# Performance work log

Hardware: AMD Instinct MI355X
Metric: run time of the kernel (lower is better)

The kernel has to match this reference:

```python
import jax, jax.numpy as jnp
import numpy as np

D = 1024
H = 16
HD = D // H  # 64
S = 2048
B = 1


def setup_inputs() -> dict:
    key = jax.random.key(0)
    ks = jax.random.split(key, 6)
    return {
        "GLO": jax.random.normal(ks[0], (B, S, D), dtype=jnp.float32),
        "LOC": jax.random.normal(ks[1], (B, S, D), dtype=jnp.float32),
        "W_q": jax.random.normal(ks[2], (H, D, HD), dtype=jnp.float32),
        "W_k": jax.random.normal(ks[3], (H, D, HD), dtype=jnp.float32),
        "W_v": jax.random.normal(ks[4], (H, D, HD), dtype=jnp.float32),
        "W_o": jax.random.normal(ks[5], (H * HD, D), dtype=jnp.float32),
    }


def _cross_attn(q_src, kv_src, W_q, W_k, W_v, W_o):
    # q_src: [B,Sq,D], kv_src: [B,Sk,D]
    b, sq, _ = q_src.shape
    Q = jnp.einsum('bsd,hde->bhse', q_src, W_q)   # [B,H,Sq,hd]
    K = jnp.einsum('bsd,hde->bhse', kv_src, W_k)  # [B,H,Sk,hd]
    V = jnp.einsum('bsd,hde->bhse', kv_src, W_v)  # [B,H,Sk,hd]
    scores = jnp.einsum('bhqe,bhke->bhqk', Q, K) / jnp.sqrt(jnp.float32(HD))
    weights = jax.nn.softmax(scores, axis=-1)
    out = jnp.einsum('bhqk,bhke->bhqe', weights, V)  # [B,H,Sq,hd]
    # Faithful to torch .view (raw memory reinterpretation, no head transpose)
    out = out.reshape(b, sq, H * HD)
    return out @ W_o  # [B,Sq,D]


def reference(GLO, LOC, W_q, W_k, W_v, W_o):
    GLO_prime = _cross_attn(GLO, LOC, W_q, W_k, W_v, W_o)
    LOC_prime = _cross_attn(LOC, GLO, W_q, W_k, W_v, W_o)
    return (GLO_prime, LOC_prime)
```

## Files before the change

### kernel.cpp

```cpp
#include <hip/hip_runtime.h>
#include <math.h>

#define S_LEN 2048
#define D_DIM 1024
#define NH 16
#define HD 64

typedef __attribute__((ext_vector_type(8))) short bf16x8;
typedef __attribute__((ext_vector_type(4))) float f32x4;

#define MFMA(a, b, c) __builtin_amdgcn_mfma_f32_16x16x32_bf16((a), (b), (c), 0, 0, 0)

__device__ __forceinline__ unsigned short f2bf(float x) {
    unsigned int u = __float_as_uint(x);
    u = (u + 0x7FFFu + ((u >> 16) & 1u)) >> 16;
    return (unsigned short)u;
}
__device__ __forceinline__ float bf2f(unsigned short b) {
    return __uint_as_float(((unsigned int)b) << 16);
}
__device__ __forceinline__ void gl_lds16(const void* g, void* l) {
    __builtin_amdgcn_global_load_lds((const __attribute__((address_space(1))) unsigned int*)g,
                                     (__attribute__((address_space(3))) unsigned int*)l, 16, 0, 0);
}


__global__ __launch_bounds__(256) void prep(const float* __restrict__ GLO,
                                            const float* __restrict__ LOC,
                                            const float* __restrict__ Wq,
                                            const float* __restrict__ Wk,
                                            const float* __restrict__ Wv,
                                            const float* __restrict__ Wo,
                                            unsigned short* __restrict__ Xh,
                                            unsigned short* __restrict__ Xl,
                                            unsigned short* __restrict__ Wqh,
                                            unsigned short* __restrict__ Wql,
                                            unsigned short* __restrict__ Wkh,
                                            unsigned short* __restrict__ Wkl,
                                            unsigned short* __restrict__ Wvt,
                                            unsigned short* __restrict__ Wot) {
    int idx = blockIdx.x * 256 + threadIdx.x;
    if (idx < (1 << 22)) {
        const float* src = (idx & (1 << 21)) ? LOC : GLO;
        float x = src[idx & ((1 << 21) - 1)];
        int r = idx >> 10;
        int k = idx & 1023;
        size_t t = (size_t)(r >> 7) * 131072 + (size_t)(k >> 6) * 8192 + (r & 127) * 64 +
                   ((((k >> 3) & 7) ^ (r & 7)) * 8) + (k & 7);
        unsigned short h = f2bf(x);
        Xh[t] = h;
        Xl[t] = f2bf(x - bf2f(h));
    } else {
        idx -= (1 << 22);
        int sec = idx >> 20;
        int i = idx & 0xFFFFF;
        if (sec < 3) {
            int e = i & 63;
            int d = (i >> 6) & 1023;
            int h = i >> 16;
            float wv = ((sec == 0) ? Wq : (sec == 1) ? Wk : Wv)[h * 65536 + d * 64 + e];
            size_t t = (size_t)h * 65536 + (size_t)(d >> 6) * 4096 + e * 64 +
                       ((((d >> 3) & 7) ^ (e & 7)) * 8) + (d & 7);
            if (sec == 0) {
                wv *= 0.18033688011112042f;
                unsigned short hi = f2bf(wv);
                Wqh[t] = hi;
                Wql[t] = f2bf(wv - bf2f(hi));
            } else if (sec == 1) {
                unsigned short hi = f2bf(wv);
                Wkh[t] = hi;
                Wkl[t] = f2bf(wv - bf2f(hi));
            } else {
                Wvt[t] = f2bf(wv);
            }
        } else {
            int n = i & 1023;
            int k = i >> 10;
            size_t t = (size_t)(n >> 6) * 65536 + (size_t)(k >> 6) * 4096 + (n & 63) * 64 +
                       ((((k >> 3) & 7) ^ (n & 7)) * 8) + (k & 7);
            Wot[t] = f2bf(Wo[k * 1024 + n]);
        }
    }
}

__global__ __launch_bounds__(256) void qkv_proj(const unsigned short* __restrict__ Xh,
                                                const unsigned short* __restrict__ Xl,
                                                const unsigned short* __restrict__ Wqh,
                                                const unsigned short* __restrict__ Wql,
                                                const unsigned short* __restrict__ Wkh,
                                                const unsigned short* __restrict__ Wkl,
                                                const unsigned short* __restrict__ Wvt,
                                                unsigned short* __restrict__ Qh,
                                                unsigned short* __restrict__ Ql,
                                                unsigned short* __restrict__ Kh,
                                                unsigned short* __restrict__ Kl,
                                                unsigned short* __restrict__ Vt) {
    __shared__ unsigned short lds[36864];
    const int bid = blockIdx.x;
    const int mblk = bid & 31;
    const int head = bid >> 5;
    const int tid = threadIdx.x;
    const int lane = tid & 63;
    const int w = tid >> 6;
    const int l15 = lane & 15, quad = lane >> 4;

    f32x4 aq[2][4] = {}, ak[2][4] = {}, av[2][4] = {};
    const size_t abase0 = (size_t)mblk * 131072;
    const size_t bbase0 = (size_t)head * 65536;

    for (int kb = 0; kb < 16; ++kb) {
        __syncthreads();
        {
            const size_t ab = abase0 + (size_t)kb * 8192;
            const size_t bb = bbase0 + (size_t)kb * 4096;
#pragma unroll
            for (int j = 0; j < 4; ++j) {
                int seg = j * 256 + tid;
                gl_lds16(Xh + ab + seg * 8, &lds[seg * 8]);
                gl_lds16(Xl + ab + seg * 8, &lds[8192 + seg * 8]);
            }
#pragma unroll
            for (int j = 0; j < 2; ++j) {
                int seg = j * 256 + tid;
                gl_lds16(Wqh + bb + seg * 8, &lds[16384 + seg * 8]);
                gl_lds16(Wql + bb + seg * 8, &lds[20480 + seg * 8]);
                gl_lds16(Wkh + bb + seg * 8, &lds[24576 + seg * 8]);
                gl_lds16(Wkl + bb + seg * 8, &lds[28672 + seg * 8]);
                gl_lds16(Wvt + bb + seg * 8, &lds[32768 + seg * 8]);
            }
        }
        __syncthreads();

#pragma unroll
        for (int ksub = 0; ksub < 2; ++ksub) {
            bf16x8 ah[2], al8[2];
#pragma unroll
            for (int mt = 0; mt < 2; ++mt) {
                int row = w * 32 + mt * 16 + l15;
                int g = (ksub * 4 + quad) ^ (row & 7);
                ah[mt] = *(const bf16x8*)&lds[row * 64 + g * 8];
                al8[mt] = *(const bf16x8*)&lds[8192 + row * 64 + g * 8];
            }
#pragma unroll
            for (int nt = 0; nt < 4; ++nt) {
                int col = nt * 16 + l15;
                int o = col * 64 + ((ksub * 4 + quad) ^ (col & 7)) * 8;
                bf16x8 bqh = *(const bf16x8*)&lds[16384 + o];
                bf16x8 bql = *(const bf16x8*)&lds[20480 + o];
                bf16x8 bkh = *(const bf16x8*)&lds[24576 + o];
                bf16x8 bkl = *(const bf16x8*)&lds[28672 + o];
                bf16x8 bv = *(const bf16x8*)&lds[32768 + o];
#pragma unroll
                for (int mt = 0; mt < 2; ++mt) {
                    f32x4 a = aq[mt][nt];
                    a = MFMA(ah[mt], bqh, a);
                    a = MFMA(ah[mt], bql, a);
                    a = MFMA(al8[mt], bqh, a);
                    aq[mt][nt] = a;
                    f32x4 b = ak[mt][nt];
                    b = MFMA(ah[mt], bkh, b);
                    b = MFMA(ah[mt], bkl, b);
                    b = MFMA(al8[mt], bkh, b);
                    ak[mt][nt] = b;
                    av[mt][nt] = MFMA(ah[mt], bv, av[mt][nt]);
                }
            }
        }
    }

#pragma unroll
    for (int mt = 0; mt < 2; ++mt) {
        const int rbase = mblk * 128 + w * 32 + mt * 16 + quad * 4;
#pragma unroll
        for (int nt = 0; nt < 4; ++nt) {
            const int col = head * 64 + nt * 16 + l15;
#pragma unroll
            for (int r = 0; r < 4; ++r) {
                size_t a = (size_t)(rbase + r) * D_DIM + col;
                float vq = aq[mt][nt][r];
                unsigned short hq = f2bf(vq);
                Qh[a] = hq;
                Ql[a] = f2bf(vq - bf2f(hq));
                float vk = ak[mt][nt][r];
                unsigned short hk = f2bf(vk);
                Kh[a] = hk;
                Kl[a] = f2bf(vk - bf2f(hk));
            }
            ushort4 vp;
            vp.x = f2bf(av[mt][nt][0]);
            vp.y = f2bf(av[mt][nt][1]);
            vp.z = f2bf(av[mt][nt][2]);
            vp.w = f2bf(av[mt][nt][3]);
            *(ushort4*)(Vt + (size_t)col * (2 * S_LEN) + rbase) = vp;
        }
    }
}

__global__ __launch_bounds__(256) void attn_kernel(const unsigned short* __restrict__ Qh_,
                                                   const unsigned short* __restrict__ Ql_,
                                                   const unsigned short* __restrict__ Kh_,
                                                   const unsigned short* __restrict__ Kl_,
                                                   const unsigned short* __restrict__ Vt_,
                                                   unsigned short* __restrict__ Oatt) {
    __shared__ unsigned short lds[21504];
    const int bid = blockIdx.x;
    const int qblk = bid & 15;
    const int head = (bid >> 4) & 15;
    const int dir = bid >> 8;
    const int src_q = dir, src_kv = 1 - dir;

    const int tid = threadIdx.x;
    const int lane = tid & 63;
    const int w = tid >> 6;
    const int l15 = lane & 15, quad = lane >> 4;
    const int q0w = qblk * 128 + w * 32;

    bf16x8 qh[2][2], ql[2][2];
#pragma unroll
    for (int mt = 0; mt < 2; ++mt) {
        const size_t qrow =
            (size_t)(src_q * S_LEN + q0w + mt * 16 + l15) * D_DIM + head * 64 + quad * 8;
#pragma unroll
        for (int c = 0; c < 2; ++c) {
            qh[mt][c] = *(const bf16x8*)(Qh_ + qrow + c * 32);
            ql[mt][c] = *(const bf16x8*)(Ql_ + qrow + c * 32);
        }
    }

    f32x4 o[2][4] = {};
    float mi[2] = {-1e30f, -1e30f}, li[2] = {0.f, 0.f};
    unsigned short* Pw = lds + 12288 + w * 2304;

    for (int k0 = 0; k0 < S_LEN; k0 += 64) {
        __syncthreads();
        {
            const unsigned short* KhB = Kh_ + (size_t)(src_kv * S_LEN + k0) * D_DIM + head * 64;
            const unsigned short* KlB = Kl_ + (size_t)(src_kv * S_LEN + k0) * D_DIM + head * 64;
            const unsigned short* VB = Vt_ + (size_t)(head * 64) * (2 * S_LEN) + src_kv * S_LEN + k0;
#pragma unroll
            for (int j = 0; j < 2; ++j) {
                int i = j * 256 + tid;
                int row = i >> 3, c16 = i & 7;
                int sc = c16 ^ (row & 7);
                gl_lds16(KhB + (size_t)row * D_DIM + sc * 8, &lds[i * 8]);
                gl_lds16(KlB + (size_t)row * D_DIM + sc * 8, &lds[4096 + i * 8]);
                gl_lds16(VB + (size_t)row * (2 * S_LEN) + sc * 8, &lds[8192 + i * 8]);
            }
        }
        __syncthreads();

        f32x4 sa[2][4];
#pragma unroll
        for (int kt = 0; kt < 4; ++kt) {
            const int row = kt * 16 + l15;
            const int s0 = (quad ^ (row & 7)) * 8;
            const int s1 = ((4 + quad) ^ (row & 7)) * 8;
            bf16x8 kh0 = *(const bf16x8*)&lds[row * 64 + s0];
            bf16x8 kh1 = *(const bf16x8*)&lds[row * 64 + s1];
            bf16x8 kl0 = *(const bf16x8*)&lds[4096 + row * 64 + s0];
            bf16x8 kl1 = *(const bf16x8*)&lds[4096 + row * 64 + s1];
#pragma unroll
            for (int mt = 0; mt < 2; ++mt) {
                f32x4 a = {};
                a = MFMA(kh0, qh[mt][0], a);
                a = MFMA(kh1, qh[mt][1], a);
                a = MFMA(kl0, qh[mt][0], a);
                a = MFMA(kl1, qh[mt][1], a);
                a = MFMA(kh0, ql[mt][0], a);
                a = MFMA(kh1, ql[mt][1], a);
                sa[mt][kt] = a;
            }
        }

#pragma unroll
        for (int mt = 0; mt < 2; ++mt) {
            f32x4 t4 = __builtin_elementwise_max(__builtin_elementwise_max(sa[mt][0], sa[mt][1]),
                                                 __builtin_elementwise_max(sa[mt][2], sa[mt][3]));
            float tm = fmaxf(fmaxf(t4[0], t4[1]), fmaxf(t4[2], t4[3]));
            tm = fmaxf(tm, __shfl_xor(tm, 16, 64));
            tm = fmaxf(tm, __shfl_xor(tm, 32, 64));
            float mn = fmaxf(mi[mt], tm);
            float al = exp2f(mi[mt] - mn);
            mi[mt] = mn;
            const f32x4 mnv = {mn, mn, mn, mn};
            f32x4 rs4 = {};
#pragma unroll
            for (int kt = 0; kt < 4; ++kt) {
                f32x4 p = sa[mt][kt] - mnv;
#pragma unroll
                for (int r = 0; r < 4; ++r) p[r] = exp2f(p[r]);
                rs4 += p;
                unsigned u0 = __float_as_uint(p[0]) + 0x8000u;
                unsigned u1 = __float_as_uint(p[1]) + 0x8000u;
                unsigned u2 = __float_as_uint(p[2]) + 0x8000u;
                unsigned u3 = __float_as_uint(p[3]) + 0x8000u;
                uint2 pk;
                pk.x = __builtin_amdgcn_perm(u1, u0, 0x07060302u);
                pk.y = __builtin_amdgcn_perm(u3, u2, 0x07060302u);
                *(uint2*)&Pw[(mt * 16 + l15) * 72 + kt * 16 + quad * 4] = pk;
            }
            float rs = (rs4[0] + rs4[1]) + (rs4[2] + rs4[3]);
            rs += __shfl_xor(rs, 16, 64);
            rs += __shfl_xor(rs, 32, 64);
            li[mt] = li[mt] * al + rs;
            const f32x4 alv = {al, al, al, al};
#pragma unroll
            for (int et = 0; et < 4; ++et) o[mt][et] *= alv;
        }

#pragma unroll
        for (int c = 0; c < 2; ++c) {
            bf16x8 pf[2];
#pragma unroll
            for (int mt = 0; mt < 2; ++mt)
                pf[mt] = *(const bf16x8*)&Pw[(mt * 16 + l15) * 72 + c * 32 + quad * 8];
#pragma unroll
            for (int et = 0; et < 4; ++et) {
                const int row = et * 16 + l15;
                const int sl = ((c * 4 + quad) ^ (row & 7)) * 8;
                bf16x8 vf = *(const bf16x8*)&lds[8192 + row * 64 + sl];
#pragma unroll
                for (int mt = 0; mt < 2; ++mt) o[mt][et] = MFMA(vf, pf[mt], o[mt][et]);
            }
        }
    }

    const size_t obase = (size_t)(dir * 16 + head) * 131072 + (size_t)l15 * 8192;
#pragma unroll
    for (int mt = 0; mt < 2; ++mt) {
        float rl = __builtin_amdgcn_rcpf(li[mt]);
        const int rowit = qblk * 8 + w * 2 + mt;
#pragma unroll
        for (int et = 0; et < 4; ++et) {
            int g = ((et * 2 + (quad >> 1)) ^ (rowit & 7)) & 7;
            ushort4 pk;
            pk.x = f2bf(o[mt][et][0] * rl);
            pk.y = f2bf(o[mt][et][1] * rl);
            pk.z = f2bf(o[mt][et][2] * rl);
            pk.w = f2bf(o[mt][et][3] * rl);
            *(ushort4*)(Oatt + obase + (size_t)rowit * 64 + g * 8 + (quad & 1) * 4) = pk;
        }
    }
}

__global__ __launch_bounds__(256) void oproj(const unsigned short* __restrict__ Oatt,
                                             const unsigned short* __restrict__ Wot,
                                             float* __restrict__ out) {
    __shared__ unsigned short lds[12288];
    const int bid = blockIdx.x;
    const int nblk = bid & 15;
    const int mblk = bid >> 4;
    const int tid = threadIdx.x;
    const int lane = tid & 63, w = tid >> 6, l15 = lane & 15, quad = lane >> 4;

    f32x4 acc[2][4] = {};
    const size_t abase = (size_t)mblk * 131072;
    const size_t bbase = (size_t)nblk * 65536;
    for (int kb = 0; kb < 16; ++kb) {
        __syncthreads();
#pragma unroll
        for (int j = 0; j < 4; ++j) {
            int seg = j * 256 + tid;
            gl_lds16(Oatt + abase + (size_t)kb * 8192 + seg * 8, &lds[seg * 8]);
        }
#pragma unroll
        for (int j = 0; j < 2; ++j) {
            int seg = j * 256 + tid;
            gl_lds16(Wot + bbase + (size_t)kb * 4096 + seg * 8, &lds[8192 + seg * 8]);
        }
        __syncthreads();
#pragma unroll
        for (int ksub = 0; ksub < 2; ++ksub) {
            bf16x8 a[2];
#pragma unroll
            for (int mt = 0; mt < 2; ++mt) {
                int row = w * 32 + mt * 16 + l15;
                a[mt] = *(const bf16x8*)&lds[row * 64 + (((ksub * 4 + quad) ^ (row & 7)) * 8)];
            }
#pragma unroll
            for (int nt = 0; nt < 4; ++nt) {
                int col = nt * 16 + l15;
                bf16x8 b =
                    *(const bf16x8*)&lds[8192 + col * 64 + (((ksub * 4 + quad) ^ (col & 7)) * 8)];
#pragma unroll
                for (int mt = 0; mt < 2; ++mt) acc[mt][nt] = MFMA(a[mt], b, acc[mt][nt]);
            }
        }
    }
#pragma unroll
    for (int mt = 0; mt < 2; ++mt) {
        const int rbase = mblk * 128 + w * 32 + mt * 16 + quad * 4;
#pragma unroll
        for (int nt = 0; nt < 4; ++nt)
#pragma unroll
            for (int r = 0; r < 4; ++r)
                out[(size_t)(rbase + r) * D_DIM + nblk * 64 + nt * 16 + l15] = acc[mt][nt][r];
    }
}

extern "C" void kernel_launch(void* const* d_in, const int* in_sizes, int n_in, void* d_out,
                              int out_size, void* d_ws, size_t ws_size, hipStream_t stream) {
    const float* GLO = (const float*)d_in[0];
    const float* LOC = (const float*)d_in[1];
    const float* Wq = (const float*)d_in[2];
    const float* Wk = (const float*)d_in[3];
    const float* Wv = (const float*)d_in[4];
    const float* Wo = (const float*)d_in[5];
    float* out = (float*)d_out;

    unsigned short* ws = (unsigned short*)d_ws;
    unsigned short* Xh = ws + 0;
    unsigned short* Xl = ws + 4194304;
    unsigned short* Wqh = ws + 8388608;
    unsigned short* Wql = ws + 9437184;
    unsigned short* Wkh = ws + 10485760;
    unsigned short* Wkl = ws + 11534336;
    unsigned short* Wvt = ws + 12582912;
    unsigned short* Wot = ws + 13631488;
    unsigned short* Qh = ws + 14680064;
    unsigned short* Ql = ws + 18874368;
    unsigned short* Kh = ws + 23068672;
    unsigned short* Kl = ws + 27262976;
    unsigned short* Vt = ws + 31457280;
    unsigned short* Oatt = ws + 35651584;

    prep<<<32768, 256, 0, stream>>>(GLO, LOC, Wq, Wk, Wv, Wo, Xh, Xl, Wqh, Wql, Wkh, Wkl, Wvt, Wot);
    qkv_proj<<<512, 256, 0, stream>>>(Xh, Xl, Wqh, Wql, Wkh, Wkl, Wvt, Qh, Ql, Kh, Kl, Vt);
    attn_kernel<<<512, 256, 0, stream>>>(Qh, Ql, Kh, Kl, Vt, Oatt);
    oproj<<<512, 256, 0, stream>>>(Oatt, Wot, out);
}
```

Baseline: 291.4 us.

## Split attention KV range across two blocks and merge partials in combine kernel

The attention grid doubles so each block handles half of the key/value sequence. Partial outputs plus the row max and sum are written to scratch buffers that reuse the Xh/Xl workspace, and a new combine kernel merges the two halves. The online-softmax rescale is now skipped when no lane's maximum grows, and the P tile in shared memory drops its padding in favour of an XOR swizzle. The split raises the block count from 512 to 1024 to improve occupancy across CUs, at the cost of an extra kernel launch, extra global traffic and an extra bf16 rounding of the partial outputs.

```diff
diff --git a/kernel.cpp b/kernel.cpp
--- a/kernel.cpp
+++ b/kernel.cpp
@@ -196,17 +196,20 @@
     }
 }
 
-__global__ __launch_bounds__(256) void attn_kernel(const unsigned short* __restrict__ Qh_,
-                                                   const unsigned short* __restrict__ Ql_,
-                                                   const unsigned short* __restrict__ Kh_,
-                                                   const unsigned short* __restrict__ Kl_,
-                                                   const unsigned short* __restrict__ Vt_,
-                                                   unsigned short* __restrict__ Oatt) {
-    __shared__ unsigned short lds[21504];
+__global__ __launch_bounds__(256, 4) void attn_kernel(const unsigned short* __restrict__ Qh_,
+                                                      const unsigned short* __restrict__ Ql_,
+                                                      const unsigned short* __restrict__ Kh_,
+                                                      const unsigned short* __restrict__ Kl_,
+                                                      const unsigned short* __restrict__ Vt_,
+                                                      unsigned short* __restrict__ Opart0,
+                                                      unsigned short* __restrict__ Opart1,
+                                                      float* __restrict__ MlL) {
+    __shared__ unsigned short lds[20480];
     const int bid = blockIdx.x;
     const int qblk = bid & 15;
     const int head = (bid >> 4) & 15;
-    const int dir = bid >> 8;
+    const int dir = (bid >> 8) & 1;
+    const int ks = bid >> 9;
     const int src_q = dir, src_kv = 1 - dir;
 
     const int tid = threadIdx.x;
@@ -229,9 +232,10 @@
 
     f32x4 o[2][4] = {};
     float mi[2] = {-1e30f, -1e30f}, li[2] = {0.f, 0.f};
-    unsigned short* Pw = lds + 12288 + w * 2304;
-
-    for (int k0 = 0; k0 < S_LEN; k0 += 64) {
+    unsigned short* Pw = lds + 12288 + w * 2048;
+
+    const int kbeg = ks * 1024;
+    for (int k0 = kbeg; k0 < kbeg + 1024; k0 += 64) {
         __syncthreads();
         {
             const unsigned short* KhB = Kh_ + (size_t)(src_kv * S_LEN + k0) * D_DIM + head * 64;
@@ -279,9 +283,16 @@
             float tm = fmaxf(fmaxf(t4[0], t4[1]), fmaxf(t4[2], t4[3]));
             tm = fmaxf(tm, __shfl_xor(tm, 16, 64));
             tm = fmaxf(tm, __shfl_xor(tm, 32, 64));
-            float mn = fmaxf(mi[mt], tm);
-            float al = exp2f(mi[mt] - mn);
-            mi[mt] = mn;
+            if (__ballot(tm > mi[mt])) {
+                float mn = fmaxf(mi[mt], tm);
+                float al = exp2f(mi[mt] - mn);
+                mi[mt] = mn;
+                li[mt] *= al;
+                const f32x4 alv = {al, al, al, al};
+#pragma unroll
+                for (int et = 0; et < 4; ++et) o[mt][et] *= alv;
+            }
+            const float mn = mi[mt];
             const f32x4 mnv = {mn, mn, mn, mn};
             f32x4 rs4 = {};
 #pragma unroll
@@ -297,15 +308,13 @@
                 uint2 pk;
                 pk.x = __builtin_amdgcn_perm(u1, u0, 0x07060302u);
                 pk.y = __builtin_amdgcn_perm(u3, u2, 0x07060302u);
-                *(uint2*)&Pw[(mt * 16 + l15) * 72 + kt * 16 + quad * 4] = pk;
+                int g = (kt * 2 + (quad >> 1)) ^ (l15 & 7);
+                *(uint2*)&Pw[(mt * 16 + l15) * 64 + g * 8 + (quad & 1) * 4] = pk;
             }
             float rs = (rs4[0] + rs4[1]) + (rs4[2] + rs4[3]);
             rs += __shfl_xor(rs, 16, 64);
             rs += __shfl_xor(rs, 32, 64);
-            li[mt] = li[mt] * al + rs;
-            const f32x4 alv = {al, al, al, al};
-#pragma unroll
-            for (int et = 0; et < 4; ++et) o[mt][et] *= alv;
+            li[mt] += rs;
         }
 
 #pragma unroll
@@ -313,7 +322,8 @@
             bf16x8 pf[2];
 #pragma unroll
             for (int mt = 0; mt < 2; ++mt)
-                pf[mt] = *(const bf16x8*)&Pw[(mt * 16 + l15) * 72 + c * 32 + quad * 8];
+                pf[mt] =
+                    *(const bf16x8*)&Pw[(mt * 16 + l15) * 64 + (((c * 4 + quad) ^ (l15 & 7)) * 8)];
 #pragma unroll
             for (int et = 0; et < 4; ++et) {
                 const int row = et * 16 + l15;
@@ -325,6 +335,7 @@
         }
     }
 
+    unsigned short* Op = ks ? Opart1 : Opart0;
     const size_t obase = (size_t)(dir * 16 + head) * 131072 + (size_t)l15 * 8192;
 #pragma unroll
     for (int mt = 0; mt < 2; ++mt) {
@@ -338,9 +349,48 @@
             pk.y = f2bf(o[mt][et][1] * rl);
             pk.z = f2bf(o[mt][et][2] * rl);
             pk.w = f2bf(o[mt][et][3] * rl);
-            *(ushort4*)(Oatt + obase + (size_t)rowit * 64 + g * 8 + (quad & 1) * 4) = pk;
-        }
-    }
+            *(ushort4*)(Op + obase + (size_t)rowit * 64 + g * 8 + (quad & 1) * 4) = pk;
+        }
+        if (quad == 0) {
+            int mli = ks * 65536 + (dir * 16 + head) * 2048 + qblk * 128 + w * 32 + mt * 16 + l15;
+            MlL[mli] = mi[mt];
+            MlL[131072 + mli] = li[mt];
+        }
+    }
+}
+
+__device__ __forceinline__ unsigned comb2(unsigned a, unsigned b, float w0, float w1) {
+    float a0 = bf2f((unsigned short)(a & 0xFFFF)), a1 = bf2f((unsigned short)(a >> 16));
+    float b0 = bf2f((unsigned short)(b & 0xFFFF)), b1 = bf2f((unsigned short)(b >> 16));
+    unsigned r0 = f2bf(a0 * w0 + b0 * w1);
+    unsigned r1 = f2bf(a1 * w0 + b1 * w1);
+    return r0 | (r1 << 16);
+}
+__global__ __launch_bounds__(256) void combine(unsigned short* __restrict__ Op0,
+                                               const unsigned short* __restrict__ Op1,
+                                               const float* __restrict__ MlL) {
+    int gl = blockIdx.x * 256 + threadIdx.x;
+    int g8 = gl & 7;
+    int q = (gl >> 3) & 2047;
+    int mh = gl >> 14;
+    size_t addr = (size_t)mh * 131072 + (size_t)(q & 15) * 8192 + (q >> 4) * 64 +
+                  ((g8 ^ ((q >> 4) & 7)) * 8);
+    int mli = mh * 2048 + q;
+    float m0 = MlL[mli], m1 = MlL[65536 + mli];
+    float l0 = MlL[131072 + mli], l1 = MlL[131072 + 65536 + mli];
+    float M = fmaxf(m0, m1);
+    float w0 = l0 * exp2f(m0 - M), w1 = l1 * exp2f(m1 - M);
+    float rw = 1.f / (w0 + w1);
+    w0 *= rw;
+    w1 *= rw;
+    uint4 a = *(const uint4*)(Op0 + addr);
+    uint4 b = *(const uint4*)(Op1 + addr);
+    uint4 r;
+    r.x = comb2(a.x, b.x, w0, w1);
+    r.y = comb2(a.y, b.y, w0, w1);
+    r.z = comb2(a.z, b.z, w0, w1);
+    r.w = comb2(a.w, b.w, w0, w1);
+    *(uint4*)(Op0 + addr) = r;
 }
 
 __global__ __launch_bounds__(256) void oproj(const unsigned short* __restrict__ Oatt,
@@ -423,9 +473,12 @@
     unsigned short* Kl = ws + 27262976;
     unsigned short* Vt = ws + 31457280;
     unsigned short* Oatt = ws + 35651584;
+    unsigned short* Opart1 = Xh;
+    float* MlL = (float*)Xl;
 
     prep<<<32768, 256, 0, stream>>>(GLO, LOC, Wq, Wk, Wv, Wo, Xh, Xl, Wqh, Wql, Wkh, Wkl, Wvt, Wot);
     qkv_proj<<<512, 256, 0, stream>>>(Xh, Xl, Wqh, Wql, Wkh, Wkl, Wvt, Qh, Ql, Kh, Kl, Vt);
-    attn_kernel<<<512, 256, 0, stream>>>(Qh, Ql, Kh, Kl, Vt, Oatt);
+    attn_kernel<<<1024, 256, 0, stream>>>(Qh, Ql, Kh, Kl, Vt, Oatt, Opart1, MlL);
+    combine<<<2048, 256, 0, stream>>>(Oatt, Opart1, MlL);
     oproj<<<512, 256, 0, stream>>>(Oatt, Wot, out);
 }
```

After: 311.5 us. 1.07x slower.

## Double-buffer K/V tiles in attention and skip redundant softmax rescales

Applied to the files above, without the earlier changes.

The attention kernel now uses two LDS buffers for the K-high, K-low and V tiles. The next 64-key tile is loaded with global_load_lds while the current tile is computed, so the loop runs two chunks per iteration with a barrier between them. The online-softmax rescale of the accumulator and row sum is skipped unless the running max actually increases anywhere in the wave. The P staging buffer is shrunk to one 16-row swizzled tile per wave that is reused for each m-tile, which keeps total LDS near 56 KB per block at the cost of fewer blocks fitting per CU.

```diff
diff --git a/kernel.cpp b/kernel.cpp
--- a/kernel.cpp
+++ b/kernel.cpp
@@ -202,7 +202,7 @@
                                                    const unsigned short* __restrict__ Kl_,
                                                    const unsigned short* __restrict__ Vt_,
                                                    unsigned short* __restrict__ Oatt) {
-    __shared__ unsigned short lds[21504];
+    __shared__ unsigned short lds[28672];
     const int bid = blockIdx.x;
     const int qblk = bid & 15;
     const int head = (bid >> 4) & 15;
@@ -215,6 +215,26 @@
     const int l15 = lane & 15, quad = lane >> 4;
     const int q0w = qblk * 128 + w * 32;
 
+    const unsigned short* KhB0 = Kh_ + (size_t)(src_kv * S_LEN) * D_DIM + head * 64;
+    const unsigned short* KlB0 = Kl_ + (size_t)(src_kv * S_LEN) * D_DIM + head * 64;
+    const unsigned short* Vtp = Vt_ + (size_t)(head * 64) * (2 * S_LEN) + src_kv * S_LEN;
+
+    const int i0 = tid, i1 = 256 + tid;
+    const int sr0 = i0 >> 3, sc0 = ((i0 & 7) ^ (sr0 & 7)) * 8;
+    const int sr1 = i1 >> 3, sc1 = ((i1 & 7) ^ (sr1 & 7)) * 8;
+
+    auto stage = [&](int k0, int boff) {
+        const unsigned short* KhB = KhB0 + (size_t)k0 * D_DIM;
+        const unsigned short* KlB = KlB0 + (size_t)k0 * D_DIM;
+        const unsigned short* VB = Vtp + k0;
+        gl_lds16(KhB + (size_t)sr0 * D_DIM + sc0, &lds[boff + i0 * 8]);
+        gl_lds16(KhB + (size_t)sr1 * D_DIM + sc1, &lds[boff + i1 * 8]);
+        gl_lds16(KlB + (size_t)sr0 * D_DIM + sc0, &lds[boff + 4096 + i0 * 8]);
+        gl_lds16(KlB + (size_t)sr1 * D_DIM + sc1, &lds[boff + 4096 + i1 * 8]);
+        gl_lds16(VB + (size_t)sr0 * (2 * S_LEN) + sc0, &lds[boff + 8192 + i0 * 8]);
+        gl_lds16(VB + (size_t)sr1 * (2 * S_LEN) + sc1, &lds[boff + 8192 + i1 * 8]);
+    };
+
     bf16x8 qh[2][2], ql[2][2];
 #pragma unroll
     for (int mt = 0; mt < 2; ++mt) {
@@ -229,36 +249,19 @@
 
     f32x4 o[2][4] = {};
     float mi[2] = {-1e30f, -1e30f}, li[2] = {0.f, 0.f};
-    unsigned short* Pw = lds + 12288 + w * 2304;
-
-    for (int k0 = 0; k0 < S_LEN; k0 += 64) {
-        __syncthreads();
-        {
-            const unsigned short* KhB = Kh_ + (size_t)(src_kv * S_LEN + k0) * D_DIM + head * 64;
-            const unsigned short* KlB = Kl_ + (size_t)(src_kv * S_LEN + k0) * D_DIM + head * 64;
-            const unsigned short* VB = Vt_ + (size_t)(head * 64) * (2 * S_LEN) + src_kv * S_LEN + k0;
-#pragma unroll
-            for (int j = 0; j < 2; ++j) {
-                int i = j * 256 + tid;
-                int row = i >> 3, c16 = i & 7;
-                int sc = c16 ^ (row & 7);
-                gl_lds16(KhB + (size_t)row * D_DIM + sc * 8, &lds[i * 8]);
-                gl_lds16(KlB + (size_t)row * D_DIM + sc * 8, &lds[4096 + i * 8]);
-                gl_lds16(VB + (size_t)row * (2 * S_LEN) + sc * 8, &lds[8192 + i * 8]);
-            }
-        }
-        __syncthreads();
-
+    unsigned short* Pw = lds + 24576 + w * 1024;
+
+    auto chunk = [&](int kb) {
         f32x4 sa[2][4];
 #pragma unroll
         for (int kt = 0; kt < 4; ++kt) {
             const int row = kt * 16 + l15;
             const int s0 = (quad ^ (row & 7)) * 8;
             const int s1 = ((4 + quad) ^ (row & 7)) * 8;
-            bf16x8 kh0 = *(const bf16x8*)&lds[row * 64 + s0];
-            bf16x8 kh1 = *(const bf16x8*)&lds[row * 64 + s1];
-            bf16x8 kl0 = *(const bf16x8*)&lds[4096 + row * 64 + s0];
-            bf16x8 kl1 = *(const bf16x8*)&lds[4096 + row * 64 + s1];
+            bf16x8 kh0 = *(const bf16x8*)&lds[kb + row * 64 + s0];
+            bf16x8 kh1 = *(const bf16x8*)&lds[kb + row * 64 + s1];
+            bf16x8 kl0 = *(const bf16x8*)&lds[kb + 4096 + row * 64 + s0];
+            bf16x8 kl1 = *(const bf16x8*)&lds[kb + 4096 + row * 64 + s1];
 #pragma unroll
             for (int mt = 0; mt < 2; ++mt) {
                 f32x4 a = {};
@@ -279,9 +282,16 @@
             float tm = fmaxf(fmaxf(t4[0], t4[1]), fmaxf(t4[2], t4[3]));
             tm = fmaxf(tm, __shfl_xor(tm, 16, 64));
             tm = fmaxf(tm, __shfl_xor(tm, 32, 64));
-            float mn = fmaxf(mi[mt], tm);
-            float al = exp2f(mi[mt] - mn);
-            mi[mt] = mn;
+            if (__ballot(tm > mi[mt])) {
+                float mn = fmaxf(mi[mt], tm);
+                float al = exp2f(mi[mt] - mn);
+                mi[mt] = mn;
+                li[mt] *= al;
+                const f32x4 alv = {al, al, al, al};
+#pragma unroll
+                for (int et = 0; et < 4; ++et) o[mt][et] *= alv;
+            }
+            const float mn = mi[mt];
             const f32x4 mnv = {mn, mn, mn, mn};
             f32x4 rs4 = {};
 #pragma unroll
@@ -297,32 +307,37 @@
                 uint2 pk;
                 pk.x = __builtin_amdgcn_perm(u1, u0, 0x07060302u);
                 pk.y = __builtin_amdgcn_perm(u3, u2, 0x07060302u);
-                *(uint2*)&Pw[(mt * 16 + l15) * 72 + kt * 16 + quad * 4] = pk;
+                int g = (kt * 2 + (quad >> 1)) ^ (l15 & 7);
+                *(uint2*)&Pw[l15 * 64 + g * 8 + (quad & 1) * 4] = pk;
             }
             float rs = (rs4[0] + rs4[1]) + (rs4[2] + rs4[3]);
             rs += __shfl_xor(rs, 16, 64);
             rs += __shfl_xor(rs, 32, 64);
-            li[mt] = li[mt] * al + rs;
-            const f32x4 alv = {al, al, al, al};
-#pragma unroll
-            for (int et = 0; et < 4; ++et) o[mt][et] *= alv;
-        }
-
-#pragma unroll
-        for (int c = 0; c < 2; ++c) {
-            bf16x8 pf[2];
-#pragma unroll
-            for (int mt = 0; mt < 2; ++mt)
-                pf[mt] = *(const bf16x8*)&Pw[(mt * 16 + l15) * 72 + c * 32 + quad * 8];
-#pragma unroll
-            for (int et = 0; et < 4; ++et) {
-                const int row = et * 16 + l15;
-                const int sl = ((c * 4 + quad) ^ (row & 7)) * 8;
-                bf16x8 vf = *(const bf16x8*)&lds[8192 + row * 64 + sl];
-#pragma unroll
-                for (int mt = 0; mt < 2; ++mt) o[mt][et] = MFMA(vf, pf[mt], o[mt][et]);
-            }
-        }
+            li[mt] += rs;
+
+#pragma unroll
+            for (int c = 0; c < 2; ++c) {
+                bf16x8 pf = *(const bf16x8*)&Pw[l15 * 64 + (((c * 4 + quad) ^ (l15 & 7)) * 8)];
+#pragma unroll
+                for (int et = 0; et < 4; ++et) {
+                    const int row = et * 16 + l15;
+                    const int sl = ((c * 4 + quad) ^ (row & 7)) * 8;
+                    bf16x8 vf = *(const bf16x8*)&lds[kb + 8192 + row * 64 + sl];
+                    o[mt][et] = MFMA(vf, pf, o[mt][et]);
+                }
+            }
+        }
+    };
+
+    stage(0, 0);
+#pragma unroll 1
+    for (int kd = 0; kd < 32; kd += 2) {
+        __syncthreads();
+        if (kd + 1 < 32) stage((kd + 1) * 64, 12288);
+        chunk(0);
+        __syncthreads();
+        if (kd + 2 < 32) stage((kd + 2) * 64, 0);
+        chunk(12288);
     }
 
     const size_t obase = (size_t)(dir * 16 + head) * 131072 + (size_t)l15 * 8192;
```

Result: faster. 277.4 us (-4.8%).
